# Performance work log

Measured on AMD Instinct MI355X. Metric: run time of the kernel, lower is better.

Reference implementation:

```python
import jax, jax.numpy as jnp
import numpy as np

VERY_NEG = -1e30

H = 768           # hidden_size
A_DIM = 768       # attention_dim_size
N_TREE = 40000    # num_tree_nodes (embed_init vocab)
N_CODES = 10000   # number of leaf codes (rows of leaves_list)
MAX_ANC = 8       # max ancestors per code
B, V, M = 16, 32, 48  # batch, visits, codes per visit
OUT = 512         # classifier output_size


def setup_inputs() -> dict:
    key = jax.random.key(0)
    ks = jax.random.split(key, 12)
    leaves_list = jax.random.randint(ks[0], (N_CODES, MAX_ANC), 0, N_TREE)
    ancestors_list = jax.random.randint(ks[1], (N_CODES, MAX_ANC), 0, N_TREE)
    masks = (jax.random.uniform(ks[2], (N_CODES, MAX_ANC)) > 0.3).astype(jnp.float32)
    masks = masks.at[:, 0].set(1.0)  # ensure at least one valid ancestor
    input_ids = jax.random.randint(ks[3], (B, V, M), 0, N_CODES + 1)  # 0 is padding row
    code_mask = (jax.random.uniform(ks[4], (B, V, M)) > 0.2).astype(jnp.float32)
    code_mask = code_mask.at[:, :, 0].set(1.0)
    s = 1.0 / np.sqrt(H)
    embed_table = jax.random.normal(ks[5], (N_TREE, H), dtype=jnp.float32) * s
    w1 = jax.random.normal(ks[6], (2 * H, A_DIM), dtype=jnp.float32) * (1.0 / np.sqrt(2 * H))
    b1 = jnp.zeros((A_DIM,), dtype=jnp.float32)
    w2 = jax.random.normal(ks[7], (A_DIM, 1), dtype=jnp.float32) * (1.0 / np.sqrt(A_DIM))
    b2 = jnp.zeros((1,), dtype=jnp.float32)
    wc = jax.random.normal(ks[8], (H, OUT), dtype=jnp.float32) * s
    bc = jnp.zeros((OUT,), dtype=jnp.float32)
    return {
        "embed_table": embed_table, "w1": w1, "b1": b1, "w2": w2, "b2": b2,
        "wc": wc, "bc": bc, "masks": masks, "code_mask": code_mask,
        "leaves_list": leaves_list, "ancestors_list": ancestors_list,
        "input_ids": input_ids,
    }


def reference(embed_table, w1, b1, w2, b2, wc, bc, masks, code_mask,
              leaves_list, ancestors_list, input_ids):
    # --- DAGAttention2D over ancestor axis ---
    leaves = embed_table[leaves_list]        # [N, A, H]
    ancestors = embed_table[ancestors_list]  # [N, A, H]
    m = masks[:, :, None]                    # [N, A, 1]
    x = jnp.concatenate([leaves * m, ancestors * m], axis=-1)  # [N, A, 2H]
    x = jax.nn.relu(jnp.einsum('nah,hd->nad', x, w1) + b1)
    x = jnp.einsum('nad,do->nao', x, w2) + b2                  # [N, A, 1]
    x = x + (1.0 - m) * VERY_NEG
    attn = jax.nn.softmax(x, axis=1)                           # softmax over ancestors
    dag_emb = (attn * ancestors * m).sum(axis=1)               # [N, H]
    # --- dict_matrix with padding row 0, embedding lookup ---
    dict_matrix = jnp.concatenate([jnp.zeros((1, dag_emb.shape[1]), dag_emb.dtype), dag_emb], axis=0)
    emb = dict_matrix[input_ids]             # [B, V, M, H]
    cm = code_mask[..., None]
    pooled = (emb * cm).sum(axis=2) / jnp.clip(cm.sum(axis=2), 1.0, None)  # [B, V, H]
    # --- Classifier (dropout inactive at eval, activation=None) ---
    out = jnp.einsum('bvh,ho->bvo', pooled, wc) + bc           # [B, V, OUT]
    return out
```

## Files before the change

### kernel.cpp

```cpp
#include <hip/hip_runtime.h>
#include <stdint.h>

typedef unsigned short u16;
typedef __bf16 bfx8 __attribute__((ext_vector_type(8)));
typedef float f32x4 __attribute__((ext_vector_type(4)));

#define HD 768
#define NTREE 40000
#define NCODES 10000
#define GNN 1536
#define OUTD 512
#define NBV 512
#define VNEG (-1e30f)
#define TB 4

#define BM 256
#define BN 256
#define BK 64
#define NKT (HD / BK)
#define NMT ((NTREE + BM - 1) / BM)
#define NNT (GNN / BN)
#define GRID (NMT * NNT)
#define Q8 (GRID / 8)
#define R8 (GRID % 8)

#define WAITV(n) asm volatile("s_waitcnt vmcnt(" #n ")" ::: "memory")
#define LGKM(n)  asm volatile("s_waitcnt lgkmcnt(" #n ")" ::: "memory")

__device__ __forceinline__ float bf2f(u16 u) {
  union { uint32_t i; float f; } v; v.i = ((uint32_t)u) << 16; return v.f;
}
__device__ __forceinline__ u16 f2bf(float f) {
  union { float fl; uint32_t i; } v; v.fl = f;
  uint32_t u = v.i;
  u += 0x7FFFu + ((u >> 16) & 1u);
  return (u16)(u >> 16);
}

__global__ void k_convE(const float* __restrict__ E, u16* __restrict__ Ebf, int n4) {
  int i = blockIdx.x * blockDim.x + threadIdx.x;
  if (i >= n4) return;
  float4 v = ((const float4*)E)[i];
  ushort4 r;
  r.x = f2bf(v.x); r.y = f2bf(v.y); r.z = f2bf(v.z); r.w = f2bf(v.w);
  ((ushort4*)Ebf)[i] = r;
}

__global__ void k_bt(const float* __restrict__ w1, u16* __restrict__ Bt) {
  int idx = blockIdx.x * blockDim.x + threadIdx.x;
  if (idx >= GNN * HD) return;
  int n = idx / HD, k = idx % HD;
  int srow = k + ((n >= HD) ? HD : 0);
  int scol = (n >= HD) ? (n - HD) : n;
  Bt[idx] = f2bf(w1[(size_t)srow * HD + scol]);
}

__global__ __launch_bounds__(512, 2) void k_gemm(const u16* __restrict__ A,
                                                 const u16* __restrict__ B,
                                                 u16* __restrict__ C) {
  __shared__ u16 lds[65536];

  const int tid    = threadIdx.x;
  const int lane   = tid & 63;
  const int wv     = tid >> 6;
  const int wm     = wv >> 2;
  const int wn2    = wv & 3;
  const int lane15 = lane & 15;
  const int g      = lane >> 4;

  const int orig = blockIdx.x;
  const int xcd = orig & 7, lin = orig >> 3;
  const int wg = (xcd < R8 ? xcd * (Q8 + 1) : R8 * (Q8 + 1) + (xcd - R8) * Q8) + lin;
  const int mt = wg / NNT, nt = wg % NNT;
  const int tm = mt * BM, tn = nt * BN;

  uint32_t aOff[2][2], bOff[2][2];
#pragma unroll
  for (int u = 0; u < 2; ++u) {
    const int o    = u * 8192 + tid * 16;
    const int rloc = o >> 7;
    const int c    = ((o >> 4) & 7) ^ (rloc & 7);
#pragma unroll
    for (int h = 0; h < 2; ++h) {
      int ra = tm + h * 128 + rloc; if (ra > NTREE - 1) ra = NTREE - 1;
      aOff[u][h] = (uint32_t)ra * HD + c * 8;
      bOff[u][h] = (uint32_t)(tn + h * 128 + rloc) * HD + c * 8;
    }
  }

#define STAGE_A(MH, NB, TT) do {                                               \
    _Pragma("unroll") for (int u = 0; u < 2; ++u)                              \
      __builtin_amdgcn_global_load_lds(                                        \
        (const __attribute__((address_space(1))) void*)(A + aOff[u][MH] + (TT) * BK), \
        (__attribute__((address_space(3))) void*)((char*)lds + (NB) * 32768 +  \
            (MH) * 16384 + u * 8192 + tid * 16),                               \
        16, 0, 0);                                                             \
  } while (0)

#define STAGE_B(NH, NB, TT) do {                                               \
    _Pragma("unroll") for (int u = 0; u < 2; ++u)                              \
      __builtin_amdgcn_global_load_lds(                                        \
        (const __attribute__((address_space(1))) void*)(B + bOff[u][NH] + (TT) * BK), \
        (__attribute__((address_space(3))) void*)((char*)lds + 65536 +         \
            (NB) * 32768 + (NH) * 16384 + u * 8192 + tid * 16),                \
        16, 0, 0);                                                             \
  } while (0)

  f32x4 acc[8][4];
#pragma unroll
  for (int i = 0; i < 8; ++i)
#pragma unroll
    for (int j = 0; j < 4; ++j) acc[i][j] = (f32x4){0.f, 0.f, 0.f, 0.f};

  int colz[2];
  colz[0] = ((0 * 4 + g) ^ (lane15 & 7)) * 8;
  colz[1] = ((1 * 4 + g) ^ (lane15 & 7)) * 8;
  const int aBase = (wm * 128 + lane15) * 64;
  const int bBase = (wn2 * 64 + lane15) * 64;

  bfx8 aF0[4], aF1[4], bF0[4], bF1[4];

#define READ_A(DST, MH, KS, BA) do {                                           \
    const int _a = (BA) + aBase + (MH) * 4096 + colz[KS];                      \
    _Pragma("unroll") for (int i = 0; i < 4; ++i)                              \
      DST[i] = *(const bfx8*)&lds[_a + i * 1024];                              \
  } while (0)

#define READ_B(DST, KS, BB) do {                                               \
    const int _b = (BB) + bBase + colz[KS];                                    \
    _Pragma("unroll") for (int j = 0; j < 4; ++j)                              \
      DST[j] = *(const bfx8*)&lds[_b + j * 1024];                              \
  } while (0)

#define MFMA16(MH, AFR, BFR) do {                                              \
    __builtin_amdgcn_s_setprio(1);                                             \
    _Pragma("unroll") for (int i = 0; i < 4; ++i)                              \
      _Pragma("unroll") for (int j = 0; j < 4; ++j)                            \
        acc[(MH) * 4 + i][j] = __builtin_amdgcn_mfma_f32_16x16x32_bf16(        \
            AFR[i], BFR[j], acc[(MH) * 4 + i][j], 0, 0, 0);                    \
    __builtin_amdgcn_s_setprio(0);                                             \
  } while (0)

  STAGE_A(0, 0, 0);
  STAGE_A(1, 0, 0);
  STAGE_B(0, 0, 0);
  STAGE_B(1, 0, 0);
  WAITV(0);
  __builtin_amdgcn_s_barrier();
  READ_A(aF0, 0, 0, 0);
  READ_B(bF0, 0, 32768);

  for (int t = 0; t < NKT; ++t) {
    const int bA  = (t & 1) * 16384;
    const int bB  = 32768 + (t & 1) * 16384;
    const int nb  = (t + 1) & 1;
    const int nbA = nb * 16384;
    const int nbB = 32768 + nb * 16384;
    const bool more = (t + 1 < NKT);

    READ_A(aF1, 1, 0, bA);
    if (more) { STAGE_A(0, nb, t + 1); STAGE_A(1, nb, t + 1); }
    LGKM(4);
    __builtin_amdgcn_sched_barrier(0);
    MFMA16(0, aF0, bF0);
    __builtin_amdgcn_s_barrier();

    READ_A(aF0, 0, 1, bA);
    READ_B(bF1, 1, bB);
    if (more) { STAGE_B(0, nb, t + 1); STAGE_B(1, nb, t + 1); }
    LGKM(8);
    __builtin_amdgcn_sched_barrier(0);
    MFMA16(1, aF1, bF0);
    __builtin_amdgcn_s_barrier();

    READ_A(aF1, 1, 1, bA);
    LGKM(4);
    __builtin_amdgcn_sched_barrier(0);
    MFMA16(0, aF0, bF1);
    WAITV(0);
    __builtin_amdgcn_s_barrier();

    if (more) {
      READ_A(aF0, 0, 0, nbA);
      READ_B(bF0, 0, nbB);
      LGKM(8);
    } else {
      LGKM(0);
    }
    __builtin_amdgcn_sched_barrier(0);
    MFMA16(1, aF1, bF1);
    __builtin_amdgcn_s_barrier();
  }

  const int r0 = (lane >> 4) * 4, cc = lane15;
#pragma unroll
  for (int mf = 0; mf < 8; ++mf) {
#pragma unroll
    for (int nf = 0; nf < 4; ++nf) {
#pragma unroll
      for (int rr = 0; rr < 4; ++rr) {
        const int row = tm + wm * 128 + mf * 16 + r0 + rr;
        if (row < NTREE) {
          const int col = tn + wn2 * 64 + nf * 16 + cc;
          C[(size_t)row * GNN + col] = f2bf(acc[mf][nf][rr]);
        }
      }
    }
  }
#undef MFMA16
#undef READ_A
#undef READ_B
#undef STAGE_A
#undef STAGE_B
}

__global__ __launch_bounds__(512) void k_attn(const u16* __restrict__ PQ,
                                              const u16* __restrict__ Ebf,
                                              const float* __restrict__ b1,
                                              const float* __restrict__ w2,
                                              const float* __restrict__ b2,
                                              const float* __restrict__ masks,
                                              const int* __restrict__ leaves,
                                              const int* __restrict__ anc,
                                              float* __restrict__ dag) {
  const int n = blockIdx.x;
  const int tid = threadIdx.x, lane = tid & 63, wv = tid >> 6;
  __shared__ float sc[8];
  __shared__ float m_s[8];
  __shared__ int   an_s[8];
  __shared__ int   lv_s[8];
  if (tid < 8) {
    an_s[tid] = anc[n * 8 + tid];
    lv_s[tid] = leaves[n * 8 + tid];
    m_s[tid]  = masks[n * 8 + tid];
  }
  __syncthreads();

  {
    const int a = wv;
    const float mm = m_s[a];
    if (mm == 0.f) {
      if (lane == 0) sc[a] = VNEG;
    } else {
      const int l = lv_s[a], an = an_s[a];
      const u16* pr = PQ + (size_t)l * GNN;
      const u16* qr = PQ + (size_t)an * GNN + HD;
      const int d0 = lane * 12;
      float s = 0.f;
#pragma unroll
      for (int jj = 0; jj < 3; ++jj) {
        const int d = d0 + jj * 4;
        ushort4 pv = *(const ushort4*)(pr + d);
        ushort4 qv = *(const ushort4*)(qr + d);
        float4  bb = *(const float4*)(b1 + d);
        float4  ww = *(const float4*)(w2 + d);
        float v;
        v = fmaxf(bf2f(pv.x) + bf2f(qv.x) + bb.x, 0.f); s += v * ww.x;
        v = fmaxf(bf2f(pv.y) + bf2f(qv.y) + bb.y, 0.f); s += v * ww.y;
        v = fmaxf(bf2f(pv.z) + bf2f(qv.z) + bb.z, 0.f); s += v * ww.z;
        v = fmaxf(bf2f(pv.w) + bf2f(qv.w) + bb.w, 0.f); s += v * ww.w;
      }
#pragma unroll
      for (int off = 32; off > 0; off >>= 1) s += __shfl_down(s, off);
      if (lane == 0) sc[a] = s + b2[0];
    }
  }
  __syncthreads();

  float mx = sc[0];
#pragma unroll
  for (int a = 1; a < 8; ++a) mx = fmaxf(mx, sc[a]);
  float ex[8], den = 0.f;
#pragma unroll
  for (int a = 0; a < 8; ++a) { ex[a] = expf(sc[a] - mx); den += ex[a]; }
  const float inv = 1.0f / den;
  float cf[8];
#pragma unroll
  for (int a = 0; a < 8; ++a) cf[a] = ex[a] * inv * m_s[a];

  {
    const int d = tid;
    float accv = 0.f;
#pragma unroll
    for (int a = 0; a < 8; ++a) {
      const float cfa = cf[a];
      if (cfa != 0.f) accv += cfa * bf2f(Ebf[(size_t)an_s[a] * HD + d]);
    }
    dag[(size_t)n * HD + d] = accv;
  }
  if (tid < 256) {
    const int d = 512 + tid;
    float accv = 0.f;
#pragma unroll
    for (int a = 0; a < 8; ++a) {
      const float cfa = cf[a];
      if (cfa != 0.f) accv += cfa * bf2f(Ebf[(size_t)an_s[a] * HD + d]);
    }
    dag[(size_t)n * HD + d] = accv;
  }
}

__global__ __launch_bounds__(256) void k_pool(const float* __restrict__ dag,
                                              const int* __restrict__ ids,
                                              const float* __restrict__ cm,
                                              float* __restrict__ pooled) {
  const int bv = blockIdx.x, tid = threadIdx.x;
  __shared__ int   id_s[48];
  __shared__ float cm_s[48];
  if (tid < 48) { id_s[tid] = ids[bv * 48 + tid]; cm_s[tid] = cm[bv * 48 + tid]; }
  __syncthreads();
  float cnt = 0.f;
  for (int m = 0; m < 48; ++m) cnt += cm_s[m];
  const float scale = 1.0f / fmaxf(cnt, 1.0f);
  if (tid < 192) {
    float4 accv = make_float4(0.f, 0.f, 0.f, 0.f);
    for (int m = 0; m < 48; ++m) {
      const int id = id_s[m];
      const float cv = cm_s[m];
      if (id > 0 && cv != 0.f) {
        float4 v = *(const float4*)(dag + (size_t)(id - 1) * HD + tid * 4);
        accv.x += cv * v.x; accv.y += cv * v.y;
        accv.z += cv * v.z; accv.w += cv * v.w;
      }
    }
    accv.x *= scale; accv.y *= scale; accv.z *= scale; accv.w *= scale;
    *(float4*)(pooled + (size_t)bv * HD + tid * 4) = accv;
  }
}

__global__ __launch_bounds__(256) void k_out(const float* __restrict__ pooled,
                                             const float* __restrict__ wc,
                                             const float* __restrict__ bc,
                                             float* __restrict__ out) {
  const int b0 = blockIdx.x * TB;
  const int tid = threadIdx.x;
  __shared__ float pl[TB][HD];
  for (int i = tid; i < TB * HD; i += 256) pl[i / HD][i % HD] = pooled[(size_t)b0 * HD + i];
  __syncthreads();
  float a0[TB], a1[TB];
#pragma unroll
  for (int r = 0; r < TB; ++r) { a0[r] = 0.f; a1[r] = 0.f; }
  for (int h = 0; h < HD; ++h) {
    const float w0  = wc[(size_t)h * OUTD + tid];
    const float w1v = wc[(size_t)h * OUTD + tid + 256];
#pragma unroll
    for (int r = 0; r < TB; ++r) { const float p = pl[r][h]; a0[r] += p * w0; a1[r] += p * w1v; }
  }
  const float bc0 = bc[tid], bc1 = bc[tid + 256];
#pragma unroll
  for (int r = 0; r < TB; ++r) {
    out[(size_t)(b0 + r) * OUTD + tid]       = a0[r] + bc0;
    out[(size_t)(b0 + r) * OUTD + tid + 256] = a1[r] + bc1;
  }
}

extern "C" void kernel_launch(void* const* d_in, const int* in_sizes, int n_in,
                              void* d_out, int out_size, void* d_ws, size_t ws_size,
                              hipStream_t stream) {
  const float* E     = (const float*)d_in[0];
  const float* w1    = (const float*)d_in[1];
  const float* b1    = (const float*)d_in[2];
  const float* w2    = (const float*)d_in[3];
  const float* b2    = (const float*)d_in[4];
  const float* wc    = (const float*)d_in[5];
  const float* bc    = (const float*)d_in[6];
  const float* masks = (const float*)d_in[7];
  const float* cm    = (const float*)d_in[8];
  const int*   leaves = (const int*)d_in[9];
  const int*   anc    = (const int*)d_in[10];
  const int*   ids    = (const int*)d_in[11];
  float* out = (float*)d_out;

  if (n_in < 12) return;
  if (in_sizes[0] != NTREE * HD) return;
  if (out_size != NBV * OUTD) return;

  char* ws = (char*)d_ws;
  const size_t szEbf = (size_t)NTREE * HD * 2;
  const size_t szBt  = (size_t)GNN * HD * 2;
  const size_t szPQ  = (size_t)NTREE * GNN * 2;
  const size_t szDag = (size_t)NCODES * HD * 4;
  const size_t szPl  = (size_t)NBV * HD * 4;
  if (ws_size < szEbf + szBt + szPQ + szDag + szPl) return;

  u16*   Ebf    = (u16*)ws;            ws += szEbf;
  u16*   Bt     = (u16*)ws;            ws += szBt;
  u16*   PQ     = (u16*)ws;            ws += szPQ;
  float* dag    = (float*)ws;          ws += szDag;
  float* pooled = (float*)ws;          ws += szPl;

  const int n4 = NTREE * HD / 4;
  k_convE<<<(n4 + 255) / 256, 256, 0, stream>>>(E, Ebf, n4);
  k_bt<<<(GNN * HD + 255) / 256, 256, 0, stream>>>(w1, Bt);
  k_gemm<<<GRID, 512, 0, stream>>>(Ebf, Bt, PQ);
  k_attn<<<NCODES, 512, 0, stream>>>(PQ, Ebf, b1, w2, b2, masks, leaves, anc, dag);
  k_pool<<<NBV, 256, 0, stream>>>(dag, ids, cm, pooled);
  k_out<<<NBV / TB, 256, 0, stream>>>(pooled, wc, bc, out);
}
```

Measured before the change: 303.0 us.

## Deepen GEMM pipeline to 4-stage BK=32 ring, fuse prep kernels, vectorize attn gather

The GEMM main loop moves from a double-buffered BK=64 scheme to a four-slot ring of BK=32 tiles with three tiles in flight and a new swizzled LDS layout, so global loads overlap more MFMA work. The two conversion kernels (embedding to bf16 and w1 transpose) are merged into one launch. The attention weighted-sum now has each thread process two bf16 values with a 32-bit load and a float2 store. The deeper pipeline adds more barriers per K step and relies on carefully chosen vmcnt waits to stay correct.

New measurement: 287.2 us. 1.06x faster.

```diff
diff --git a/kernel.cpp b/kernel.cpp
--- a/kernel.cpp
+++ b/kernel.cpp
@@ -16,8 +16,8 @@
 
 #define BM 256
 #define BN 256
-#define BK 64
-#define NKT (HD / BK)
+#define BK2 32
+#define NKT2 (HD / BK2)
 #define NMT ((NTREE + BM - 1) / BM)
 #define NNT (GNN / BN)
 #define GRID (NMT * NNT)
@@ -37,22 +37,25 @@
   return (u16)(u >> 16);
 }
 
-__global__ void k_convE(const float* __restrict__ E, u16* __restrict__ Ebf, int n4) {
-  int i = blockIdx.x * blockDim.x + threadIdx.x;
-  if (i >= n4) return;
-  float4 v = ((const float4*)E)[i];
-  ushort4 r;
-  r.x = f2bf(v.x); r.y = f2bf(v.y); r.z = f2bf(v.z); r.w = f2bf(v.w);
-  ((ushort4*)Ebf)[i] = r;
-}
-
-__global__ void k_bt(const float* __restrict__ w1, u16* __restrict__ Bt) {
-  int idx = blockIdx.x * blockDim.x + threadIdx.x;
-  if (idx >= GNN * HD) return;
-  int n = idx / HD, k = idx % HD;
-  int srow = k + ((n >= HD) ? HD : 0);
-  int scol = (n >= HD) ? (n - HD) : n;
-  Bt[idx] = f2bf(w1[(size_t)srow * HD + scol]);
+#define NBLK_CONV 30000
+__global__ void k_prep(const float* __restrict__ E, u16* __restrict__ Ebf,
+                       const float* __restrict__ w1, u16* __restrict__ Bt) {
+  const int bid = blockIdx.x, tid = threadIdx.x;
+  if (bid < NBLK_CONV) {
+    const int i = bid * 256 + tid;
+    float4 v = ((const float4*)E)[i];
+    ushort4 r;
+    r.x = f2bf(v.x); r.y = f2bf(v.y); r.z = f2bf(v.z); r.w = f2bf(v.w);
+    ((ushort4*)Ebf)[i] = r;
+  } else {
+    const int idx = (bid - NBLK_CONV) * 256 + tid;
+    if (idx < GNN * HD) {
+      const int n = idx / HD, k = idx % HD;
+      const int srow = k + ((n >= HD) ? HD : 0);
+      const int scol = (n >= HD) ? (n - HD) : n;
+      Bt[idx] = f2bf(w1[(size_t)srow * HD + scol]);
+    }
+  }
 }
 
 __global__ __launch_bounds__(512, 2) void k_gemm(const u16* __restrict__ A,
@@ -74,122 +77,104 @@
   const int mt = wg / NNT, nt = wg % NNT;
   const int tm = mt * BM, tn = nt * BN;
 
-  uint32_t aOff[2][2], bOff[2][2];
+  uint32_t aOff[2], bOff[2];
 #pragma unroll
   for (int u = 0; u < 2; ++u) {
-    const int o    = u * 8192 + tid * 16;
-    const int rloc = o >> 7;
-    const int c    = ((o >> 4) & 7) ^ (rloc & 7);
-#pragma unroll
-    for (int h = 0; h < 2; ++h) {
-      int ra = tm + h * 128 + rloc; if (ra > NTREE - 1) ra = NTREE - 1;
-      aOff[u][h] = (uint32_t)ra * HD + c * 8;
-      bOff[u][h] = (uint32_t)(tn + h * 128 + rloc) * HD + c * 8;
-    }
-  }
-
-#define STAGE_A(MH, NB, TT) do {                                               \
-    _Pragma("unroll") for (int u = 0; u < 2; ++u)                              \
+    const int idx  = u * 512 + tid;
+    const int s    = idx >> 3;
+    const int phys = idx & 7;
+    const int slot = phys ^ (s & 7);
+    const int row  = 2 * s + (slot >> 2);
+    const int chnk = slot & 3;
+    int ra = tm + row; if (ra > NTREE - 1) ra = NTREE - 1;
+    aOff[u] = (uint32_t)ra * HD + chnk * 8;
+    bOff[u] = (uint32_t)(tn + row) * HD + chnk * 8;
+  }
+
+#define STAGE(TT) do {                                                         \
+    const int _b = ((TT) & 3);                                                 \
+    _Pragma("unroll") for (int u = 0; u < 2; ++u) {                            \
       __builtin_amdgcn_global_load_lds(                                        \
-        (const __attribute__((address_space(1))) void*)(A + aOff[u][MH] + (TT) * BK), \
-        (__attribute__((address_space(3))) void*)((char*)lds + (NB) * 32768 +  \
-            (MH) * 16384 + u * 8192 + tid * 16),                               \
-        16, 0, 0);                                                             \
+        (const __attribute__((address_space(1))) void*)(A + aOff[u] + (TT) * BK2), \
+        (__attribute__((address_space(3))) void*)((char*)lds + _b * 16384 +    \
+            u * 8192 + tid * 16), 16, 0, 0);                                   \
+      __builtin_amdgcn_global_load_lds(                                        \
+        (const __attribute__((address_space(1))) void*)(B + bOff[u] + (TT) * BK2), \
+        (__attribute__((address_space(3))) void*)((char*)lds + 65536 +         \
+            _b * 16384 + u * 8192 + tid * 16), 16, 0, 0);                      \
+    }                                                                          \
   } while (0)
 
-#define STAGE_B(NH, NB, TT) do {                                               \
-    _Pragma("unroll") for (int u = 0; u < 2; ++u)                              \
-      __builtin_amdgcn_global_load_lds(                                        \
-        (const __attribute__((address_space(1))) void*)(B + bOff[u][NH] + (TT) * BK), \
-        (__attribute__((address_space(3))) void*)((char*)lds + 65536 +         \
-            (NB) * 32768 + (NH) * 16384 + u * 8192 + tid * 16),                \
-        16, 0, 0);                                                             \
-  } while (0)
-
   f32x4 acc[8][4];
 #pragma unroll
   for (int i = 0; i < 8; ++i)
 #pragma unroll
     for (int j = 0; j < 4; ++j) acc[i][j] = (f32x4){0.f, 0.f, 0.f, 0.f};
 
-  int colz[2];
-  colz[0] = ((0 * 4 + g) ^ (lane15 & 7)) * 8;
-  colz[1] = ((1 * 4 + g) ^ (lane15 & 7)) * 8;
-  const int aBase = (wm * 128 + lane15) * 64;
-  const int bBase = (wn2 * 64 + lane15) * 64;
-
-  bfx8 aF0[4], aF1[4], bF0[4], bF1[4];
-
-#define READ_A(DST, MH, KS, BA) do {                                           \
-    const int _a = (BA) + aBase + (MH) * 4096 + colz[KS];                      \
-    _Pragma("unroll") for (int i = 0; i < 4; ++i)                              \
-      DST[i] = *(const bfx8*)&lds[_a + i * 1024];                              \
-  } while (0)
-
-#define READ_B(DST, KS, BB) do {                                               \
-    const int _b = (BB) + bBase + colz[KS];                                    \
-    _Pragma("unroll") for (int j = 0; j < 4; ++j)                              \
-      DST[j] = *(const bfx8*)&lds[_b + j * 1024];                              \
-  } while (0)
-
-#define MFMA16(MH, AFR, BFR) do {                                              \
+  int aIdx[8], bIdx[4];
+#pragma unroll
+  for (int mf = 0; mf < 8; ++mf) {
+    const int R = wm * 128 + mf * 16 + lane15;
+    const int s = R >> 1, slot = ((R & 1) << 2) | g, phys = slot ^ (s & 7);
+    aIdx[mf] = s * 64 + phys * 8;
+  }
+#pragma unroll
+  for (int nf = 0; nf < 4; ++nf) {
+    const int R = wn2 * 64 + nf * 16 + lane15;
+    const int s = R >> 1, slot = ((R & 1) << 2) | g, phys = slot ^ (s & 7);
+    bIdx[nf] = s * 64 + phys * 8;
+  }
+
+  bfx8 aX[4], aY[4], bE[4], bO[4];
+
+#define MFMA4x4(ACC0, AFR, BFR) do {                                           \
     __builtin_amdgcn_s_setprio(1);                                             \
     _Pragma("unroll") for (int i = 0; i < 4; ++i)                              \
       _Pragma("unroll") for (int j = 0; j < 4; ++j)                            \
-        acc[(MH) * 4 + i][j] = __builtin_amdgcn_mfma_f32_16x16x32_bf16(        \
-            AFR[i], BFR[j], acc[(MH) * 4 + i][j], 0, 0, 0);                    \
+        acc[(ACC0) + i][j] = __builtin_amdgcn_mfma_f32_16x16x32_bf16(          \
+            AFR[i], BFR[j], acc[(ACC0) + i][j], 0, 0, 0);                      \
     __builtin_amdgcn_s_setprio(0);                                             \
   } while (0)
 
-  STAGE_A(0, 0, 0);
-  STAGE_A(1, 0, 0);
-  STAGE_B(0, 0, 0);
-  STAGE_B(1, 0, 0);
-  WAITV(0);
+#define TILE(T, BCUR, BNXT) {                                                  \
+    const int bufA = ((T) & 3) * 8192;                                         \
+    _Pragma("unroll") for (int i = 0; i < 4; ++i)                              \
+      aY[i] = *(const bfx8*)&lds[bufA + aIdx[4 + i]];                          \
+    if ((T) + 3 < NKT2) STAGE((T) + 3);                                        \
+    LGKM(4);                                                                   \
+    __builtin_amdgcn_sched_barrier(0);                                         \
+    MFMA4x4(0, aX, BCUR);                                                      \
+    __builtin_amdgcn_s_barrier();                                              \
+    if ((T) < NKT2 - 1) {                                                      \
+      if ((T) <= NKT2 - 4)      { WAITV(8); }                                  \
+      else if ((T) == NKT2 - 3) { WAITV(4); }                                  \
+      else                      { WAITV(0); }                                  \
+      const int nA = (((T) + 1) & 3) * 8192;                                   \
+      const int nB = 32768 + (((T) + 1) & 3) * 8192;                           \
+      _Pragma("unroll") for (int i = 0; i < 4; ++i)                            \
+        aX[i] = *(const bfx8*)&lds[nA + aIdx[i]];                              \
+      _Pragma("unroll") for (int j = 0; j < 4; ++j)                            \
+        BNXT[j] = *(const bfx8*)&lds[nB + bIdx[j]];                            \
+      LGKM(8);                                                                 \
+    } else { LGKM(0); }                                                        \
+    __builtin_amdgcn_sched_barrier(0);                                         \
+    MFMA4x4(4, aY, BCUR);                                                      \
+    __builtin_amdgcn_s_barrier();                                              \
+  }
+
+  STAGE(0);
+  STAGE(1);
+  STAGE(2);
+  WAITV(8);
   __builtin_amdgcn_s_barrier();
-  READ_A(aF0, 0, 0, 0);
-  READ_B(bF0, 0, 32768);
-
-  for (int t = 0; t < NKT; ++t) {
-    const int bA  = (t & 1) * 16384;
-    const int bB  = 32768 + (t & 1) * 16384;
-    const int nb  = (t + 1) & 1;
-    const int nbA = nb * 16384;
-    const int nbB = 32768 + nb * 16384;
-    const bool more = (t + 1 < NKT);
-
-    READ_A(aF1, 1, 0, bA);
-    if (more) { STAGE_A(0, nb, t + 1); STAGE_A(1, nb, t + 1); }
-    LGKM(4);
-    __builtin_amdgcn_sched_barrier(0);
-    MFMA16(0, aF0, bF0);
-    __builtin_amdgcn_s_barrier();
-
-    READ_A(aF0, 0, 1, bA);
-    READ_B(bF1, 1, bB);
-    if (more) { STAGE_B(0, nb, t + 1); STAGE_B(1, nb, t + 1); }
-    LGKM(8);
-    __builtin_amdgcn_sched_barrier(0);
-    MFMA16(1, aF1, bF0);
-    __builtin_amdgcn_s_barrier();
-
-    READ_A(aF1, 1, 1, bA);
-    LGKM(4);
-    __builtin_amdgcn_sched_barrier(0);
-    MFMA16(0, aF0, bF1);
-    WAITV(0);
-    __builtin_amdgcn_s_barrier();
-
-    if (more) {
-      READ_A(aF0, 0, 0, nbA);
-      READ_B(bF0, 0, nbB);
-      LGKM(8);
-    } else {
-      LGKM(0);
-    }
-    __builtin_amdgcn_sched_barrier(0);
-    MFMA16(1, aF1, bF1);
-    __builtin_amdgcn_s_barrier();
+#pragma unroll
+  for (int i = 0; i < 4; ++i) aX[i] = *(const bfx8*)&lds[aIdx[i]];
+#pragma unroll
+  for (int j = 0; j < 4; ++j) bE[j] = *(const bfx8*)&lds[32768 + bIdx[j]];
+
+  for (int t2 = 0; t2 < NKT2; t2 += 2) {
+    TILE(t2, bE, bO);
+    TILE(t2 + 1, bO, bE);
   }
 
   const int r0 = (lane >> 4) * 4, cc = lane15;
@@ -207,11 +192,9 @@
       }
     }
   }
-#undef MFMA16
-#undef READ_A
-#undef READ_B
-#undef STAGE_A
-#undef STAGE_B
+#undef TILE
+#undef MFMA4x4
+#undef STAGE
 }
 
 __global__ __launch_bounds__(512) void k_attn(const u16* __restrict__ PQ,
@@ -278,25 +261,20 @@
 #pragma unroll
   for (int a = 0; a < 8; ++a) cf[a] = ex[a] * inv * m_s[a];
 
-  {
-    const int d = tid;
-    float accv = 0.f;
+  if (tid < 384) {
+    const int d = tid * 2;
+    float a0 = 0.f, a1 = 0.f;
 #pragma unroll
     for (int a = 0; a < 8; ++a) {
       const float cfa = cf[a];
-      if (cfa != 0.f) accv += cfa * bf2f(Ebf[(size_t)an_s[a] * HD + d]);
-    }
-    dag[(size_t)n * HD + d] = accv;
-  }
-  if (tid < 256) {
-    const int d = 512 + tid;
-    float accv = 0.f;
-#pragma unroll
-    for (int a = 0; a < 8; ++a) {
-      const float cfa = cf[a];
-      if (cfa != 0.f) accv += cfa * bf2f(Ebf[(size_t)an_s[a] * HD + d]);
-    }
-    dag[(size_t)n * HD + d] = accv;
+      if (cfa != 0.f) {
+        const uint32_t w = *(const uint32_t*)(Ebf + (size_t)an_s[a] * HD + d);
+        a0 += cfa * bf2f((u16)(w & 0xffffu));
+        a1 += cfa * bf2f((u16)(w >> 16));
+      }
+    }
+    float2 r; r.x = a0; r.y = a1;
+    *(float2*)(dag + (size_t)n * HD + d) = r;
   }
 }
 
@@ -389,9 +367,8 @@
   float* dag    = (float*)ws;          ws += szDag;
   float* pooled = (float*)ws;          ws += szPl;
 
-  const int n4 = NTREE * HD / 4;
-  k_convE<<<(n4 + 255) / 256, 256, 0, stream>>>(E, Ebf, n4);
-  k_bt<<<(GNN * HD + 255) / 256, 256, 0, stream>>>(w1, Bt);
+  const int nPrep = NBLK_CONV + (GNN * HD + 255) / 256;
+  k_prep<<<nPrep, 256, 0, stream>>>(E, Ebf, w1, Bt);
   k_gemm<<<GRID, 512, 0, stream>>>(Ebf, Bt, PQ);
   k_attn<<<NCODES, 512, 0, stream>>>(PQ, Ebf, b1, w2, b2, masks, leaves, anc, dag);
   k_pool<<<NBV, 256, 0, stream>>>(dag, ids, cm, pooled);
```

## Rework GEMM into quadrant pipeline, fuse prep kernels, store dag as bf16

Applied to the files above, without the earlier changes.

Merges the fp32-to-bf16 conversion of the embedding table and the w1 transpose into one launch. Restructures the bf16 GEMM so each wave computes four 64x32 quadrants, with finer-grained staging of A/B halves interleaved between MFMA phases and partial vmcnt waits. The attention output buffer is stored as bf16 with packed 2-element loads and stores, and the pooling kernel reads bf16, halving that intermediate's traffic. The full lgkmcnt(0) waits before each MFMA block may reduce LDS/compute overlap, and bf16 dag adds rounding error.

Result: faster. 277.0 us (-8.6%).

```diff
diff --git a/kernel.cpp b/kernel.cpp
--- a/kernel.cpp
+++ b/kernel.cpp
@@ -37,22 +37,25 @@
   return (u16)(u >> 16);
 }
 
-__global__ void k_convE(const float* __restrict__ E, u16* __restrict__ Ebf, int n4) {
-  int i = blockIdx.x * blockDim.x + threadIdx.x;
-  if (i >= n4) return;
-  float4 v = ((const float4*)E)[i];
-  ushort4 r;
-  r.x = f2bf(v.x); r.y = f2bf(v.y); r.z = f2bf(v.z); r.w = f2bf(v.w);
-  ((ushort4*)Ebf)[i] = r;
-}
-
-__global__ void k_bt(const float* __restrict__ w1, u16* __restrict__ Bt) {
-  int idx = blockIdx.x * blockDim.x + threadIdx.x;
-  if (idx >= GNN * HD) return;
-  int n = idx / HD, k = idx % HD;
-  int srow = k + ((n >= HD) ? HD : 0);
-  int scol = (n >= HD) ? (n - HD) : n;
-  Bt[idx] = f2bf(w1[(size_t)srow * HD + scol]);
+#define NBLK_CONV 30000
+__global__ void k_prep(const float* __restrict__ E, u16* __restrict__ Ebf,
+                       const float* __restrict__ w1, u16* __restrict__ Bt) {
+  const int bid = blockIdx.x, tid = threadIdx.x;
+  if (bid < NBLK_CONV) {
+    const int i = bid * 256 + tid;
+    float4 v = ((const float4*)E)[i];
+    ushort4 r;
+    r.x = f2bf(v.x); r.y = f2bf(v.y); r.z = f2bf(v.z); r.w = f2bf(v.w);
+    ((ushort4*)Ebf)[i] = r;
+  } else {
+    const int idx = (bid - NBLK_CONV) * 256 + tid;
+    if (idx < GNN * HD) {
+      const int n = idx / HD, k = idx % HD;
+      const int srow = k + ((n >= HD) ? HD : 0);
+      const int scol = (n >= HD) ? (n - HD) : n;
+      Bt[idx] = f2bf(w1[(size_t)srow * HD + scol]);
+    }
+  }
 }
 
 __global__ __launch_bounds__(512, 2) void k_gemm(const u16* __restrict__ A,
@@ -63,8 +66,8 @@
   const int tid    = threadIdx.x;
   const int lane   = tid & 63;
   const int wv     = tid >> 6;
-  const int wm     = wv >> 2;
-  const int wn2    = wv & 3;
+  const int wr     = wv >> 2;
+  const int wc     = wv & 3;
   const int lane15 = lane & 15;
   const int g      = lane >> 4;
 
@@ -106,108 +109,106 @@
         16, 0, 0);                                                             \
   } while (0)
 
-  f32x4 acc[8][4];
-#pragma unroll
-  for (int i = 0; i < 8; ++i)
-#pragma unroll
-    for (int j = 0; j < 4; ++j) acc[i][j] = (f32x4){0.f, 0.f, 0.f, 0.f};
+  f32x4 acc[4][4][2];
+#pragma unroll
+  for (int q = 0; q < 4; ++q)
+#pragma unroll
+    for (int i = 0; i < 4; ++i)
+#pragma unroll
+      for (int j = 0; j < 2; ++j) acc[q][i][j] = (f32x4){0.f, 0.f, 0.f, 0.f};
 
   int colz[2];
   colz[0] = ((0 * 4 + g) ^ (lane15 & 7)) * 8;
   colz[1] = ((1 * 4 + g) ^ (lane15 & 7)) * 8;
-  const int aBase = (wm * 128 + lane15) * 64;
-  const int bBase = (wn2 * 64 + lane15) * 64;
-
-  bfx8 aF0[4], aF1[4], bF0[4], bF1[4];
-
-#define READ_A(DST, MH, KS, BA) do {                                           \
-    const int _a = (BA) + aBase + (MH) * 4096 + colz[KS];                      \
-    _Pragma("unroll") for (int i = 0; i < 4; ++i)                              \
-      DST[i] = *(const bfx8*)&lds[_a + i * 1024];                              \
-  } while (0)
-
-#define READ_B(DST, KS, BB) do {                                               \
-    const int _b = (BB) + bBase + colz[KS];                                    \
-    _Pragma("unroll") for (int j = 0; j < 4; ++j)                              \
-      DST[j] = *(const bfx8*)&lds[_b + j * 1024];                              \
-  } while (0)
-
-#define MFMA16(MH, AFR, BFR) do {                                              \
+  const int aLane = wr * 4096 + lane15 * 64;
+  const int bLane = wc * 2048 + lane15 * 64;
+
+  bfx8 aF[4][2], bF[2][2];
+
+#define READ_A(MH, BA) do {                                                    \
+    _Pragma("unroll") for (int mf = 0; mf < 4; ++mf)                           \
+      _Pragma("unroll") for (int ks = 0; ks < 2; ++ks)                         \
+        aF[mf][ks] = *(const bfx8*)&lds[(BA) + (MH) * 8192 + aLane +           \
+                                        mf * 1024 + colz[ks]];                 \
+  } while (0)
+
+#define READ_B(NH, BB) do {                                                    \
+    _Pragma("unroll") for (int nf = 0; nf < 2; ++nf)                           \
+      _Pragma("unroll") for (int ks = 0; ks < 2; ++ks)                         \
+        bF[nf][ks] = *(const bfx8*)&lds[(BB) + (NH) * 8192 + bLane +           \
+                                        nf * 1024 + colz[ks]];                 \
+  } while (0)
+
+#define MFMA_Q(Q) do {                                                         \
+    LGKM(0);                                                                   \
+    __builtin_amdgcn_sched_barrier(0);                                         \
     __builtin_amdgcn_s_setprio(1);                                             \
-    _Pragma("unroll") for (int i = 0; i < 4; ++i)                              \
-      _Pragma("unroll") for (int j = 0; j < 4; ++j)                            \
-        acc[(MH) * 4 + i][j] = __builtin_amdgcn_mfma_f32_16x16x32_bf16(        \
-            AFR[i], BFR[j], acc[(MH) * 4 + i][j], 0, 0, 0);                    \
+    _Pragma("unroll") for (int mf = 0; mf < 4; ++mf)                           \
+      _Pragma("unroll") for (int nf = 0; nf < 2; ++nf)                         \
+        _Pragma("unroll") for (int ks = 0; ks < 2; ++ks)                       \
+          acc[Q][mf][nf] = __builtin_amdgcn_mfma_f32_16x16x32_bf16(            \
+              aF[mf][ks], bF[nf][ks], acc[Q][mf][nf], 0, 0, 0);                \
     __builtin_amdgcn_s_setprio(0);                                             \
   } while (0)
 
   STAGE_A(0, 0, 0);
-  STAGE_A(1, 0, 0);
   STAGE_B(0, 0, 0);
   STAGE_B(1, 0, 0);
-  WAITV(0);
+  STAGE_A(1, 0, 0);
+  WAITV(4);
   __builtin_amdgcn_s_barrier();
-  READ_A(aF0, 0, 0, 0);
-  READ_B(bF0, 0, 32768);
 
   for (int t = 0; t < NKT; ++t) {
-    const int bA  = (t & 1) * 16384;
-    const int bB  = 32768 + (t & 1) * 16384;
-    const int nb  = (t + 1) & 1;
-    const int nbA = nb * 16384;
-    const int nbB = 32768 + nb * 16384;
+    const int bA = (t & 1) * 16384;
+    const int bB = 32768 + (t & 1) * 16384;
+    const int nb = (t + 1) & 1;
     const bool more = (t + 1 < NKT);
 
-    READ_A(aF1, 1, 0, bA);
-    if (more) { STAGE_A(0, nb, t + 1); STAGE_A(1, nb, t + 1); }
-    LGKM(4);
-    __builtin_amdgcn_sched_barrier(0);
-    MFMA16(0, aF0, bF0);
+    READ_A(0, bA);
+    READ_B(0, bB);
+    if (more) STAGE_A(0, nb, t + 1);
+    MFMA_Q(0);
+    if (more) { WAITV(4); } else { WAITV(2); }
     __builtin_amdgcn_s_barrier();
 
-    READ_A(aF0, 0, 1, bA);
-    READ_B(bF1, 1, bB);
-    if (more) { STAGE_B(0, nb, t + 1); STAGE_B(1, nb, t + 1); }
-    LGKM(8);
-    __builtin_amdgcn_sched_barrier(0);
-    MFMA16(1, aF1, bF0);
+    READ_B(1, bB);
+    if (more) STAGE_B(0, nb, t + 1);
+    MFMA_Q(1);
+    if (more) { WAITV(4); } else { WAITV(0); }
     __builtin_amdgcn_s_barrier();
 
-    READ_A(aF1, 1, 1, bA);
-    LGKM(4);
-    __builtin_amdgcn_sched_barrier(0);
-    MFMA16(0, aF0, bF1);
-    WAITV(0);
+    READ_A(1, bA);
+    if (more) STAGE_B(1, nb, t + 1);
+    MFMA_Q(2);
     __builtin_amdgcn_s_barrier();
 
-    if (more) {
-      READ_A(aF0, 0, 0, nbA);
-      READ_B(bF0, 0, nbB);
-      LGKM(8);
-    } else {
-      LGKM(0);
-    }
-    __builtin_amdgcn_sched_barrier(0);
-    MFMA16(1, aF1, bF1);
+    READ_B(0, bB);
+    if (more) STAGE_A(1, nb, t + 1);
+    MFMA_Q(3);
+    if (more) { WAITV(4); }
     __builtin_amdgcn_s_barrier();
   }
 
   const int r0 = (lane >> 4) * 4, cc = lane15;
-#pragma unroll
-  for (int mf = 0; mf < 8; ++mf) {
-#pragma unroll
-    for (int nf = 0; nf < 4; ++nf) {
-#pragma unroll
-      for (int rr = 0; rr < 4; ++rr) {
-        const int row = tm + wm * 128 + mf * 16 + r0 + rr;
-        if (row < NTREE) {
-          const int col = tn + wn2 * 64 + nf * 16 + cc;
-          C[(size_t)row * GNN + col] = f2bf(acc[mf][nf][rr]);
+  const int qmh[4] = {0, 0, 1, 1}, qnh[4] = {0, 1, 1, 0};
+#pragma unroll
+  for (int q = 0; q < 4; ++q) {
+#pragma unroll
+    for (int mf = 0; mf < 4; ++mf) {
+#pragma unroll
+      for (int nf = 0; nf < 2; ++nf) {
+#pragma unroll
+        for (int rr = 0; rr < 4; ++rr) {
+          const int row = tm + qmh[q] * 128 + wr * 64 + mf * 16 + r0 + rr;
+          if (row < NTREE) {
+            const int col = tn + qnh[q] * 128 + wc * 32 + nf * 16 + cc;
+            C[(size_t)row * GNN + col] = f2bf(acc[q][mf][nf][rr]);
+          }
         }
       }
     }
   }
-#undef MFMA16
+#undef MFMA_Q
 #undef READ_A
 #undef READ_B
 #undef STAGE_A
@@ -222,7 +223,7 @@
                                               const float* __restrict__ masks,
                                               const int* __restrict__ leaves,
                                               const int* __restrict__ anc,
-                                              float* __restrict__ dag) {
+                                              u16* __restrict__ dag) {
   const int n = blockIdx.x;
   const int tid = threadIdx.x, lane = tid & 63, wv = tid >> 6;
   __shared__ float sc[8];
@@ -278,29 +279,24 @@
 #pragma unroll
   for (int a = 0; a < 8; ++a) cf[a] = ex[a] * inv * m_s[a];
 
-  {
-    const int d = tid;
-    float accv = 0.f;
+  if (tid < 384) {
+    const int d = tid * 2;
+    float a0 = 0.f, a1 = 0.f;
 #pragma unroll
     for (int a = 0; a < 8; ++a) {
       const float cfa = cf[a];
-      if (cfa != 0.f) accv += cfa * bf2f(Ebf[(size_t)an_s[a] * HD + d]);
-    }
-    dag[(size_t)n * HD + d] = accv;
-  }
-  if (tid < 256) {
-    const int d = 512 + tid;
-    float accv = 0.f;
-#pragma unroll
-    for (int a = 0; a < 8; ++a) {
-      const float cfa = cf[a];
-      if (cfa != 0.f) accv += cfa * bf2f(Ebf[(size_t)an_s[a] * HD + d]);
-    }
-    dag[(size_t)n * HD + d] = accv;
-  }
-}
-
-__global__ __launch_bounds__(256) void k_pool(const float* __restrict__ dag,
+      if (cfa != 0.f) {
+        const uint32_t w = *(const uint32_t*)(Ebf + (size_t)an_s[a] * HD + d);
+        a0 += cfa * bf2f((u16)(w & 0xffffu));
+        a1 += cfa * bf2f((u16)(w >> 16));
+      }
+    }
+    const uint32_t packed = (uint32_t)f2bf(a0) | ((uint32_t)f2bf(a1) << 16);
+    *(uint32_t*)(dag + (size_t)n * HD + d) = packed;
+  }
+}
+
+__global__ __launch_bounds__(256) void k_pool(const u16* __restrict__ dag,
                                               const int* __restrict__ ids,
                                               const float* __restrict__ cm,
                                               float* __restrict__ pooled) {
@@ -318,9 +314,9 @@
       const int id = id_s[m];
       const float cv = cm_s[m];
       if (id > 0 && cv != 0.f) {
-        float4 v = *(const float4*)(dag + (size_t)(id - 1) * HD + tid * 4);
-        accv.x += cv * v.x; accv.y += cv * v.y;
-        accv.z += cv * v.z; accv.w += cv * v.w;
+        ushort4 v = *(const ushort4*)(dag + (size_t)(id - 1) * HD + tid * 4);
+        accv.x += cv * bf2f(v.x); accv.y += cv * bf2f(v.y);
+        accv.z += cv * bf2f(v.z); accv.w += cv * bf2f(v.w);
       }
     }
     accv.x *= scale; accv.y *= scale; accv.z *= scale; accv.w *= scale;
@@ -379,19 +375,18 @@
   const size_t szEbf = (size_t)NTREE * HD * 2;
   const size_t szBt  = (size_t)GNN * HD * 2;
   const size_t szPQ  = (size_t)NTREE * GNN * 2;
-  const size_t szDag = (size_t)NCODES * HD * 4;
+  const size_t szDag = (size_t)NCODES * HD * 2;
   const size_t szPl  = (size_t)NBV * HD * 4;
   if (ws_size < szEbf + szBt + szPQ + szDag + szPl) return;
 
   u16*   Ebf    = (u16*)ws;            ws += szEbf;
   u16*   Bt     = (u16*)ws;            ws += szBt;
   u16*   PQ     = (u16*)ws;            ws += szPQ;
-  float* dag    = (float*)ws;          ws += szDag;
+  u16*   dag    = (u16*)ws;            ws += szDag;
   float* pooled = (float*)ws;          ws += szPl;
 
-  const int n4 = NTREE * HD / 4;
-  k_convE<<<(n4 + 255) / 256, 256, 0, stream>>>(E, Ebf, n4);
-  k_bt<<<(GNN * HD + 255) / 256, 256, 0, stream>>>(w1, Bt);
+  const int nPrep = NBLK_CONV + (GNN * HD + 255) / 256;
+  k_prep<<<nPrep, 256, 0, stream>>>(E, Ebf, w1, Bt);
   k_gemm<<<GRID, 512, 0, stream>>>(Ebf, Bt, PQ);
   k_attn<<<NCODES, 512, 0, stream>>>(PQ, Ebf, b1, w2, b2, masks, leaves, anc, dag);
   k_pool<<<NBV, 256, 0, stream>>>(dag, ids, cm, pooled);
```

## Fuse prep kernels, store dag in bf16, prefetch ancestor rows, tile classifier GEMM

Applied to the files above, without the earlier changes.

Merges the two conversion kernels into a single launch. The attention kernel now prefetches the ancestor embedding rows into registers before the score phase, uses wider vector loads for PQ, and writes dag_emb as packed bf16, which halves the dag traffic. The pooling kernel uses branchless weighted loads, and the classifier becomes an LDS-tiled 64x64 GEMM. Storing dag in bf16 adds rounding error, and the register prefetch raises register pressure.

Result: faster. 269.0 us (-11.2%).

```diff
diff --git a/kernel.cpp b/kernel.cpp
--- a/kernel.cpp
+++ b/kernel.cpp
@@ -4,6 +4,7 @@
 typedef unsigned short u16;
 typedef __bf16 bfx8 __attribute__((ext_vector_type(8)));
 typedef float f32x4 __attribute__((ext_vector_type(4)));
+typedef u16 u16x8 __attribute__((ext_vector_type(8)));
 
 #define HD 768
 #define NTREE 40000
@@ -12,7 +13,6 @@
 #define OUTD 512
 #define NBV 512
 #define VNEG (-1e30f)
-#define TB 4
 
 #define BM 256
 #define BN 256
@@ -37,22 +37,25 @@
   return (u16)(u >> 16);
 }
 
-__global__ void k_convE(const float* __restrict__ E, u16* __restrict__ Ebf, int n4) {
-  int i = blockIdx.x * blockDim.x + threadIdx.x;
-  if (i >= n4) return;
-  float4 v = ((const float4*)E)[i];
-  ushort4 r;
-  r.x = f2bf(v.x); r.y = f2bf(v.y); r.z = f2bf(v.z); r.w = f2bf(v.w);
-  ((ushort4*)Ebf)[i] = r;
-}
-
-__global__ void k_bt(const float* __restrict__ w1, u16* __restrict__ Bt) {
-  int idx = blockIdx.x * blockDim.x + threadIdx.x;
-  if (idx >= GNN * HD) return;
-  int n = idx / HD, k = idx % HD;
-  int srow = k + ((n >= HD) ? HD : 0);
-  int scol = (n >= HD) ? (n - HD) : n;
-  Bt[idx] = f2bf(w1[(size_t)srow * HD + scol]);
+#define NBLK_CONV 30000
+__global__ void k_prep(const float* __restrict__ E, u16* __restrict__ Ebf,
+                       const float* __restrict__ w1, u16* __restrict__ Bt) {
+  const int bid = blockIdx.x, tid = threadIdx.x;
+  if (bid < NBLK_CONV) {
+    const int i = bid * 256 + tid;
+    float4 v = ((const float4*)E)[i];
+    ushort4 r;
+    r.x = f2bf(v.x); r.y = f2bf(v.y); r.z = f2bf(v.z); r.w = f2bf(v.w);
+    ((ushort4*)Ebf)[i] = r;
+  } else {
+    const int idx = (bid - NBLK_CONV) * 256 + tid;
+    if (idx < GNN * HD) {
+      const int n = idx / HD, k = idx % HD;
+      const int srow = k + ((n >= HD) ? HD : 0);
+      const int scol = (n >= HD) ? (n - HD) : n;
+      Bt[idx] = f2bf(w1[(size_t)srow * HD + scol]);
+    }
+  }
 }
 
 __global__ __launch_bounds__(512, 2) void k_gemm(const u16* __restrict__ A,
@@ -222,106 +225,110 @@
                                               const float* __restrict__ masks,
                                               const int* __restrict__ leaves,
                                               const int* __restrict__ anc,
-                                              float* __restrict__ dag) {
+                                              u16* __restrict__ dag) {
   const int n = blockIdx.x;
   const int tid = threadIdx.x, lane = tid & 63, wv = tid >> 6;
   __shared__ float sc[8];
   __shared__ float m_s[8];
-  __shared__ int   an_s[8];
-  __shared__ int   lv_s[8];
-  if (tid < 8) {
-    an_s[tid] = anc[n * 8 + tid];
-    lv_s[tid] = leaves[n * 8 + tid];
-    m_s[tid]  = masks[n * 8 + tid];
+
+  int anreg[8];
+#pragma unroll
+  for (int a = 0; a < 8; ++a) anreg[a] = anc[n * 8 + a];
+
+  uint32_t ew[8];
+  if (tid < 384) {
+    const int d = tid * 2;
+#pragma unroll
+    for (int a = 0; a < 8; ++a)
+      ew[a] = *(const uint32_t*)(Ebf + (size_t)anreg[a] * HD + d);
+  }
+
+  {
+    const float mm = masks[n * 8 + wv];
+    if (lane == 0) m_s[wv] = mm;
+    if (mm == 0.f) {
+      if (lane == 0) sc[wv] = VNEG;
+    } else {
+      const int l = leaves[n * 8 + wv];
+      const u16* pr = PQ + (size_t)l * GNN;
+      const u16* qr = PQ + (size_t)anreg[wv] * GNN + HD;
+      u16x8  p1 = *(const u16x8*)(pr + lane * 8);
+      u16x8  q1 = *(const u16x8*)(qr + lane * 8);
+      ushort4 p2 = *(const ushort4*)(pr + 512 + lane * 4);
+      ushort4 q2 = *(const ushort4*)(qr + 512 + lane * 4);
+      const float4 bbA = *(const float4*)(b1 + lane * 8);
+      const float4 bbB = *(const float4*)(b1 + lane * 8 + 4);
+      const float4 bbC = *(const float4*)(b1 + 512 + lane * 4);
+      const float4 wwA = *(const float4*)(w2 + lane * 8);
+      const float4 wwB = *(const float4*)(w2 + lane * 8 + 4);
+      const float4 wwC = *(const float4*)(w2 + 512 + lane * 4);
+      float s = 0.f, v;
+      v = fmaxf(bf2f(p1[0]) + bf2f(q1[0]) + bbA.x, 0.f); s += v * wwA.x;
+      v = fmaxf(bf2f(p1[1]) + bf2f(q1[1]) + bbA.y, 0.f); s += v * wwA.y;
+      v = fmaxf(bf2f(p1[2]) + bf2f(q1[2]) + bbA.z, 0.f); s += v * wwA.z;
+      v = fmaxf(bf2f(p1[3]) + bf2f(q1[3]) + bbA.w, 0.f); s += v * wwA.w;
+      v = fmaxf(bf2f(p1[4]) + bf2f(q1[4]) + bbB.x, 0.f); s += v * wwB.x;
+      v = fmaxf(bf2f(p1[5]) + bf2f(q1[5]) + bbB.y, 0.f); s += v * wwB.y;
+      v = fmaxf(bf2f(p1[6]) + bf2f(q1[6]) + bbB.z, 0.f); s += v * wwB.z;
+      v = fmaxf(bf2f(p1[7]) + bf2f(q1[7]) + bbB.w, 0.f); s += v * wwB.w;
+      v = fmaxf(bf2f(p2.x) + bf2f(q2.x) + bbC.x, 0.f);   s += v * wwC.x;
+      v = fmaxf(bf2f(p2.y) + bf2f(q2.y) + bbC.y, 0.f);   s += v * wwC.y;
+      v = fmaxf(bf2f(p2.z) + bf2f(q2.z) + bbC.z, 0.f);   s += v * wwC.z;
+      v = fmaxf(bf2f(p2.w) + bf2f(q2.w) + bbC.w, 0.f);   s += v * wwC.w;
+#pragma unroll
+      for (int off = 32; off > 0; off >>= 1) s += __shfl_down(s, off);
+      if (lane == 0) sc[wv] = s + b2[0];
+    }
   }
   __syncthreads();
 
-  {
-    const int a = wv;
-    const float mm = m_s[a];
-    if (mm == 0.f) {
-      if (lane == 0) sc[a] = VNEG;
-    } else {
-      const int l = lv_s[a], an = an_s[a];
-      const u16* pr = PQ + (size_t)l * GNN;
-      const u16* qr = PQ + (size_t)an * GNN + HD;
-      const int d0 = lane * 12;
-      float s = 0.f;
-#pragma unroll
-      for (int jj = 0; jj < 3; ++jj) {
-        const int d = d0 + jj * 4;
-        ushort4 pv = *(const ushort4*)(pr + d);
-        ushort4 qv = *(const ushort4*)(qr + d);
-        float4  bb = *(const float4*)(b1 + d);
-        float4  ww = *(const float4*)(w2 + d);
-        float v;
-        v = fmaxf(bf2f(pv.x) + bf2f(qv.x) + bb.x, 0.f); s += v * ww.x;
-        v = fmaxf(bf2f(pv.y) + bf2f(qv.y) + bb.y, 0.f); s += v * ww.y;
-        v = fmaxf(bf2f(pv.z) + bf2f(qv.z) + bb.z, 0.f); s += v * ww.z;
-        v = fmaxf(bf2f(pv.w) + bf2f(qv.w) + bb.w, 0.f); s += v * ww.w;
-      }
-#pragma unroll
-      for (int off = 32; off > 0; off >>= 1) s += __shfl_down(s, off);
-      if (lane == 0) sc[a] = s + b2[0];
-    }
-  }
-  __syncthreads();
-
-  float mx = sc[0];
-#pragma unroll
-  for (int a = 1; a < 8; ++a) mx = fmaxf(mx, sc[a]);
-  float ex[8], den = 0.f;
-#pragma unroll
-  for (int a = 0; a < 8; ++a) { ex[a] = expf(sc[a] - mx); den += ex[a]; }
-  const float inv = 1.0f / den;
-  float cf[8];
-#pragma unroll
-  for (int a = 0; a < 8; ++a) cf[a] = ex[a] * inv * m_s[a];
-
-  {
-    const int d = tid;
-    float accv = 0.f;
+  if (tid < 384) {
+    float mx = sc[0];
+#pragma unroll
+    for (int a = 1; a < 8; ++a) mx = fmaxf(mx, sc[a]);
+    float ex[8], den = 0.f;
+#pragma unroll
+    for (int a = 0; a < 8; ++a) { ex[a] = expf(sc[a] - mx); den += ex[a]; }
+    const float inv = 1.0f / den;
+    float a0 = 0.f, a1 = 0.f;
 #pragma unroll
     for (int a = 0; a < 8; ++a) {
-      const float cfa = cf[a];
-      if (cfa != 0.f) accv += cfa * bf2f(Ebf[(size_t)an_s[a] * HD + d]);
-    }
-    dag[(size_t)n * HD + d] = accv;
-  }
-  if (tid < 256) {
-    const int d = 512 + tid;
-    float accv = 0.f;
-#pragma unroll
-    for (int a = 0; a < 8; ++a) {
-      const float cfa = cf[a];
-      if (cfa != 0.f) accv += cfa * bf2f(Ebf[(size_t)an_s[a] * HD + d]);
-    }
-    dag[(size_t)n * HD + d] = accv;
-  }
-}
-
-__global__ __launch_bounds__(256) void k_pool(const float* __restrict__ dag,
+      const float cfa = ex[a] * inv * m_s[a];
+      a0 += cfa * bf2f((u16)(ew[a] & 0xffffu));
+      a1 += cfa * bf2f((u16)(ew[a] >> 16));
+    }
+    const uint32_t packed = (uint32_t)f2bf(a0) | ((uint32_t)f2bf(a1) << 16);
+    *(uint32_t*)(dag + (size_t)n * HD + tid * 2) = packed;
+  }
+}
+
+__global__ __launch_bounds__(256) void k_pool(const u16* __restrict__ dag,
                                               const int* __restrict__ ids,
                                               const float* __restrict__ cm,
                                               float* __restrict__ pooled) {
   const int bv = blockIdx.x, tid = threadIdx.x;
-  __shared__ int   id_s[48];
+  __shared__ int   ix_s[48];
+  __shared__ float w_s[48];
   __shared__ float cm_s[48];
-  if (tid < 48) { id_s[tid] = ids[bv * 48 + tid]; cm_s[tid] = cm[bv * 48 + tid]; }
+  if (tid < 48) {
+    const int id = ids[bv * 48 + tid];
+    const float cv = cm[bv * 48 + tid];
+    cm_s[tid] = cv;
+    ix_s[tid] = (id > 0) ? (id - 1) : 0;
+    w_s[tid]  = (id > 0) ? cv : 0.f;
+  }
   __syncthreads();
   float cnt = 0.f;
   for (int m = 0; m < 48; ++m) cnt += cm_s[m];
   const float scale = 1.0f / fmaxf(cnt, 1.0f);
   if (tid < 192) {
     float4 accv = make_float4(0.f, 0.f, 0.f, 0.f);
+#pragma unroll 4
     for (int m = 0; m < 48; ++m) {
-      const int id = id_s[m];
-      const float cv = cm_s[m];
-      if (id > 0 && cv != 0.f) {
-        float4 v = *(const float4*)(dag + (size_t)(id - 1) * HD + tid * 4);
-        accv.x += cv * v.x; accv.y += cv * v.y;
-        accv.z += cv * v.z; accv.w += cv * v.w;
-      }
+      const float w = w_s[m];
+      ushort4 v = *(const ushort4*)(dag + (size_t)ix_s[m] * HD + tid * 4);
+      accv.x += w * bf2f(v.x); accv.y += w * bf2f(v.y);
+      accv.z += w * bf2f(v.z); accv.w += w * bf2f(v.w);
     }
     accv.x *= scale; accv.y *= scale; accv.z *= scale; accv.w *= scale;
     *(float4*)(pooled + (size_t)bv * HD + tid * 4) = accv;
@@ -332,25 +339,53 @@
                                              const float* __restrict__ wc,
                                              const float* __restrict__ bc,
                                              float* __restrict__ out) {
-  const int b0 = blockIdx.x * TB;
+  const int rb = blockIdx.x >> 3, cb = blockIdx.x & 7;
   const int tid = threadIdx.x;
-  __shared__ float pl[TB][HD];
-  for (int i = tid; i < TB * HD; i += 256) pl[i / HD][i % HD] = pooled[(size_t)b0 * HD + i];
-  __syncthreads();
-  float a0[TB], a1[TB];
-#pragma unroll
-  for (int r = 0; r < TB; ++r) { a0[r] = 0.f; a1[r] = 0.f; }
-  for (int h = 0; h < HD; ++h) {
-    const float w0  = wc[(size_t)h * OUTD + tid];
-    const float w1v = wc[(size_t)h * OUTD + tid + 256];
-#pragma unroll
-    for (int r = 0; r < TB; ++r) { const float p = pl[r][h]; a0[r] += p * w0; a1[r] += p * w1v; }
-  }
-  const float bc0 = bc[tid], bc1 = bc[tid + 256];
-#pragma unroll
-  for (int r = 0; r < TB; ++r) {
-    out[(size_t)(b0 + r) * OUTD + tid]       = a0[r] + bc0;
-    out[(size_t)(b0 + r) * OUTD + tid + 256] = a1[r] + bc1;
+  const int ty = tid >> 4, tx = tid & 15;
+  __shared__ float pl[64][33];
+  __shared__ float wcs[32][64];
+  float acc[4][4];
+#pragma unroll
+  for (int i = 0; i < 4; ++i)
+#pragma unroll
+    for (int j = 0; j < 4; ++j) acc[i][j] = 0.f;
+
+  for (int kt = 0; kt < HD / 32; ++kt) {
+    __syncthreads();
+#pragma unroll
+    for (int u = 0; u < 2; ++u) {
+      const int i = u * 256 + tid;
+      const int r = i >> 3, kq = (i & 7) * 4;
+      float4 v = *(const float4*)(pooled + (size_t)(rb * 64 + r) * HD + kt * 32 + kq);
+      pl[r][kq] = v.x; pl[r][kq + 1] = v.y; pl[r][kq + 2] = v.z; pl[r][kq + 3] = v.w;
+    }
+#pragma unroll
+    for (int u = 0; u < 2; ++u) {
+      const int i = u * 256 + tid;
+      const int k = i >> 4, cq = (i & 15) * 4;
+      *(float4*)&wcs[k][cq] =
+          *(const float4*)(wc + (size_t)(kt * 32 + k) * OUTD + cb * 64 + cq);
+    }
+    __syncthreads();
+#pragma unroll 8
+    for (int k = 0; k < 32; ++k) {
+      const float a0 = pl[ty * 4 + 0][k], a1 = pl[ty * 4 + 1][k];
+      const float a2 = pl[ty * 4 + 2][k], a3 = pl[ty * 4 + 3][k];
+      const float4 b = *(const float4*)&wcs[k][tx * 4];
+      acc[0][0] += a0 * b.x; acc[0][1] += a0 * b.y; acc[0][2] += a0 * b.z; acc[0][3] += a0 * b.w;
+      acc[1][0] += a1 * b.x; acc[1][1] += a1 * b.y; acc[1][2] += a1 * b.z; acc[1][3] += a1 * b.w;
+      acc[2][0] += a2 * b.x; acc[2][1] += a2 * b.y; acc[2][2] += a2 * b.z; acc[2][3] += a2 * b.w;
+      acc[3][0] += a3 * b.x; acc[3][1] += a3 * b.y; acc[3][2] += a3 * b.z; acc[3][3] += a3 * b.w;
+    }
+  }
+#pragma unroll
+  for (int i = 0; i < 4; ++i) {
+#pragma unroll
+    for (int j = 0; j < 4; ++j) {
+      const int row = rb * 64 + ty * 4 + i;
+      const int col = cb * 64 + tx * 4 + j;
+      out[(size_t)row * OUTD + col] = acc[i][j] + bc[col];
+    }
   }
 }
 
@@ -379,21 +414,20 @@
   const size_t szEbf = (size_t)NTREE * HD * 2;
   const size_t szBt  = (size_t)GNN * HD * 2;
   const size_t szPQ  = (size_t)NTREE * GNN * 2;
-  const size_t szDag = (size_t)NCODES * HD * 4;
+  const size_t szDag = (size_t)NCODES * HD * 2;
   const size_t szPl  = (size_t)NBV * HD * 4;
   if (ws_size < szEbf + szBt + szPQ + szDag + szPl) return;
 
   u16*   Ebf    = (u16*)ws;            ws += szEbf;
   u16*   Bt     = (u16*)ws;            ws += szBt;
   u16*   PQ     = (u16*)ws;            ws += szPQ;
-  float* dag    = (float*)ws;          ws += szDag;
+  u16*   dag    = (u16*)ws;            ws += szDag;
   float* pooled = (float*)ws;          ws += szPl;
 
-  const int n4 = NTREE * HD / 4;
-  k_convE<<<(n4 + 255) / 256, 256, 0, stream>>>(E, Ebf, n4);
-  k_bt<<<(GNN * HD + 255) / 256, 256, 0, stream>>>(w1, Bt);
+  const int nPrep = NBLK_CONV + (GNN * HD + 255) / 256;
+  k_prep<<<nPrep, 256, 0, stream>>>(E, Ebf, w1, Bt);
   k_gemm<<<GRID, 512, 0, stream>>>(Ebf, Bt, PQ);
   k_attn<<<NCODES, 512, 0, stream>>>(PQ, Ebf, b1, w2, b2, masks, leaves, anc, dag);
   k_pool<<<NBV, 256, 0, stream>>>(dag, ids, cm, pooled);
-  k_out<<<NBV / TB, 256, 0, stream>>>(pooled, wc, bc, out);
-}
+  k_out<<<64, 256, 0, stream>>>(pooled, wc, bc, out);
+}
```
